# Kernel tuning notes

Measured on AMD Instinct MI355X. Metric: run time of the kernel, lower is better.

## Reference

```python
import jax, jax.numpy as jnp
import numpy as np

NUM_NODES = 4096
IN_DIM = 16
HIDDEN = 64
OUT_DIM = 32
HEADS = 4
NEG_SLOPE = 0.2
NEG_INF = -1e9


def _glorot(key, shape):
    fan_in, fan_out = shape[0], shape[-1]
    lim = jnp.sqrt(6.0 / (fan_in + fan_out))
    return jax.random.uniform(key, shape, jnp.float32, -lim, lim)


def setup_inputs() -> dict:
    key = jax.random.key(0)
    ks = jax.random.split(key, 8)
    B = 2
    return {
        "x": jax.random.normal(ks[0], (B, NUM_NODES, IN_DIM), jnp.float32),
        "embedding": _glorot(ks[1], (NUM_NODES, HIDDEN)),
        "W_proj": _glorot(ks[2], (IN_DIM, HIDDEN)),
        "b_proj": jnp.zeros((HIDDEN,), jnp.float32),
        "W1": _glorot(ks[3], (HIDDEN, HIDDEN)),  # heads=4, 16 per head, concat -> 64
        "att1_src": _glorot(ks[4], (HEADS, HIDDEN // HEADS)),
        "att1_dst": _glorot(ks[5], (HEADS, HIDDEN // HEADS)),
        "b1": jnp.zeros((HIDDEN,), jnp.float32),
        "W2": _glorot(ks[6], (HIDDEN, OUT_DIM)),  # heads=4, 8 per head, concat -> 32
        "att2_src": _glorot(ks[7], (HEADS, OUT_DIM // HEADS)),
        "att2_dst": _glorot(jax.random.fold_in(key, 99), (HEADS, OUT_DIM // HEADS)),
        "b2": jnp.zeros((OUT_DIM,), jnp.float32),
    }


def _gat(x, mask, W, a_src, a_dst, b):
    """Dense masked GAT layer. x: [B,N,Fin], mask: [N,N] bool (shared over batch).

    Equivalent to GATConv over edge list tf.where(adj > 0.5): for each target i,
    softmax over neighbors j of LeakyReLU(a_dst.Wh_i + a_src.Wh_j), aggregate Wh_j.
    """
    B, N, _ = x.shape
    H, F = a_src.shape
    h = (x @ W).reshape(B, N, H, F)                       # [B,N,H,F]
    s_src = jnp.einsum('bnhf,hf->bnh', h, a_src)          # per-source score
    s_dst = jnp.einsum('bnhf,hf->bnh', h, a_dst)          # per-target score
    e = s_dst[:, :, None, :] + s_src[:, None, :, :]       # [B,i,j,H]
    e = jnp.where(e > 0, e, NEG_SLOPE * e)                # LeakyReLU(0.2)
    e = jnp.where(mask[None, :, :, None], e, NEG_INF)
    alpha = jax.nn.softmax(e, axis=2)                     # softmax over neighbors j
    out = jnp.einsum('bijh,bjhf->bihf', alpha, h).reshape(B, N, H * F)
    return out + b


def reference(x, embedding, W_proj, b_proj, W1, att1_src, att1_dst, b1,
              W2, att2_src, att2_dst, b2):
    # AdaptiveAdjacency: cosine similarity of l2-normalized node embeddings
    ne = embedding / jnp.linalg.norm(embedding, axis=-1, keepdims=True)
    adj = ne @ ne.T                                       # [N,N], same for all batch
    mask = adj > 0.5                                      # edge set (incl. self-loops)

    h = x @ W_proj + b_proj                               # Dense proj -> hidden
    h = jax.nn.relu(_gat(h, mask, W1, att1_src, att1_dst, b1))
    return _gat(h, mask, W2, att2_src, att2_dst, b2)
```

## Files before the change

### kernel.cpp

```cpp
#include <hip/hip_runtime.h>
#include <hip/hip_bf16.h>
#include <stdint.h>

#define N_NODES 4096
#define BATCH 2

typedef __attribute__((ext_vector_type(8))) short short8v;
typedef __attribute__((ext_vector_type(4))) unsigned short ushort4v;
typedef __attribute__((ext_vector_type(4))) float f32x4;

#define GLL16(gsrc, ldst) \
    __builtin_amdgcn_global_load_lds((const __attribute__((address_space(1))) void*)(gsrc), \
                                     (__attribute__((address_space(3))) void*)(ldst), 16, 0, 0)

static __device__ inline unsigned short f2bf_rn(float x) {
    unsigned u = __float_as_uint(x);
    unsigned r = (u + 0x7FFFu + ((u >> 16) & 1u)) >> 16;
    return (unsigned short)r;
}
static __device__ inline float bf2f(unsigned short b) {
    return __uint_as_float(((unsigned)b) << 16);
}
static __device__ inline float rl(float v, int k) {
    return __uint_as_float(__builtin_amdgcn_readlane(__float_as_uint(v), k));
}

__global__ __launch_bounds__(256) void k1_kernel(
        const float* __restrict__ emb,
        unsigned short* __restrict__ ne_hi, unsigned short* __restrict__ ne_lo,
        const float* __restrict__ x, const float* __restrict__ Wp,
        const float* __restrict__ bp, const float* __restrict__ W1,
        const float* __restrict__ a1s, const float* __restrict__ a1d,
        float* __restrict__ h1out, float* __restrict__ ssrc, float* __restrict__ sdst) {
    int t = threadIdx.x;
    if (blockIdx.x < 256) {
        int row = blockIdx.x * 16 + (t >> 4);
        int l16 = t & 15;
        float4 v = *(const float4*)&emb[(size_t)row * 64 + l16 * 4];
        float s = v.x * v.x + v.y * v.y + v.z * v.z + v.w * v.w;
#pragma unroll
        for (int m = 8; m >= 1; m >>= 1) s += __shfl_xor(s, m);
        float inv = 1.f / sqrtf(s);
        float n0 = v.x * inv, n1 = v.y * inv, n2 = v.z * inv, n3 = v.w * inv;
        ushort4v h = {f2bf_rn(n0), f2bf_rn(n1), f2bf_rn(n2), f2bf_rn(n3)};
        ushort4v lo = {f2bf_rn(n0 - bf2f(h.x)), f2bf_rn(n1 - bf2f(h.y)),
                       f2bf_rn(n2 - bf2f(h.z)), f2bf_rn(n3 - bf2f(h.w))};
        *(ushort4v*)&ne_hi[(size_t)row * 64 + l16 * 4] = h;
        *(ushort4v*)&ne_lo[(size_t)row * 64 + l16 * 4] = lo;
    } else {
        int b = blockIdx.x - 256;
        int w = t >> 6, l = t & 63;
        int row0 = b * 32 + w * 8;

        float xv[8];
#pragma unroll
        for (int r = 0; r < 8; ++r) xv[r] = x[(size_t)(row0 + r) * 16 + (l & 15)];

        float h0[8];
        float bpv = bp[l];
#pragma unroll
        for (int r = 0; r < 8; ++r) h0[r] = bpv;
#pragma unroll
        for (int k = 0; k < 16; ++k) {
            float wk = Wp[k * 64 + l];
#pragma unroll
            for (int r = 0; r < 8; ++r) h0[r] += rl(xv[r], k) * wk;
        }

        float h1[8] = {0.f, 0.f, 0.f, 0.f, 0.f, 0.f, 0.f, 0.f};
#pragma unroll
        for (int k = 0; k < 64; ++k) {
            float wk = W1[k * 64 + l];
#pragma unroll
            for (int r = 0; r < 8; ++r) h1[r] += rl(h0[r], k) * wk;
        }

        float as_ = a1s[l], ad_ = a1d[l];
#pragma unroll
        for (int r = 0; r < 8; ++r) {
            h1out[(size_t)(row0 + r) * 64 + l] = h1[r];
            float ps = h1[r] * as_, pd = h1[r] * ad_;
#pragma unroll
            for (int m = 8; m >= 1; m >>= 1) {
                ps += __shfl_xor(ps, m);
                pd += __shfl_xor(pd, m);
            }
            if ((l & 15) == 0) {
                ssrc[(size_t)(row0 + r) * 4 + (l >> 4)] = ps;
                sdst[(size_t)(row0 + r) * 4 + (l >> 4)] = pd;
            }
        }
    }
}

__global__ __launch_bounds__(256) void adj_mfma_kernel(
        const unsigned short* __restrict__ hi, const unsigned short* __restrict__ lo,
        unsigned long long* __restrict__ mask) {
    __shared__ unsigned short Ah[128 * 64];
    __shared__ unsigned short Al[128 * 64];
    __shared__ unsigned short Bh[128 * 64];
    __shared__ unsigned short Bl[128 * 64];
    int t = threadIdx.x;
    int w = t >> 6, l = t & 63;
    int i0 = blockIdx.y * 128, j0 = blockIdx.x * 128;

    int cr = l >> 3;
    int slot = (l & 7) ^ cr;
#pragma unroll
    for (int q = 0; q < 4; ++q) {
        int lr = w * 32 + q * 8;
        size_t ga = (size_t)(i0 + lr + cr) * 64 + slot * 8;
        size_t gb = (size_t)(j0 + lr + cr) * 64 + slot * 8;
        GLL16(hi + ga, &Ah[lr * 64]);
        GLL16(lo + ga, &Al[lr * 64]);
        GLL16(hi + gb, &Bh[lr * 64]);
        GLL16(lo + gb, &Bl[lr * 64]);
    }
    __syncthreads();

    int fr = l & 15;
    int s0 = l >> 4;
    int r7 = l & 7;
    short8v aH[2][2], aL[2][2];
#pragma unroll
    for (int rt = 0; rt < 2; ++rt) {
        int base = (w * 32 + rt * 16 + fr) * 64;
        aH[rt][0] = *(const short8v*)&Ah[base + ((s0 ^ r7) << 3)];
        aH[rt][1] = *(const short8v*)&Ah[base + (((s0 + 4) ^ r7) << 3)];
        aL[rt][0] = *(const short8v*)&Al[base + ((s0 ^ r7) << 3)];
        aL[rt][1] = *(const short8v*)&Al[base + (((s0 + 4) ^ r7) << 3)];
    }

    f32x4 acc[2][8];
#pragma unroll
    for (int rt = 0; rt < 2; ++rt)
#pragma unroll
        for (int js = 0; js < 8; ++js) acc[rt][js] = (f32x4){0.f, 0.f, 0.f, 0.f};

#pragma unroll
    for (int js = 0; js < 8; ++js) {
        int bbase = (js * 16 + fr) * 64;
        short8v bH0 = *(const short8v*)&Bh[bbase + ((s0 ^ r7) << 3)];
        short8v bH1 = *(const short8v*)&Bh[bbase + (((s0 + 4) ^ r7) << 3)];
        short8v bL0 = *(const short8v*)&Bl[bbase + ((s0 ^ r7) << 3)];
        short8v bL1 = *(const short8v*)&Bl[bbase + (((s0 + 4) ^ r7) << 3)];
#pragma unroll
        for (int rt = 0; rt < 2; ++rt) {
            f32x4 a = acc[rt][js];
            a = __builtin_amdgcn_mfma_f32_16x16x32_bf16(aH[rt][0], bH0, a, 0, 0, 0);
            a = __builtin_amdgcn_mfma_f32_16x16x32_bf16(aH[rt][1], bH1, a, 0, 0, 0);
            a = __builtin_amdgcn_mfma_f32_16x16x32_bf16(aH[rt][0], bL0, a, 0, 0, 0);
            a = __builtin_amdgcn_mfma_f32_16x16x32_bf16(aH[rt][1], bL1, a, 0, 0, 0);
            a = __builtin_amdgcn_mfma_f32_16x16x32_bf16(aL[rt][0], bH0, a, 0, 0, 0);
            a = __builtin_amdgcn_mfma_f32_16x16x32_bf16(aL[rt][1], bH1, a, 0, 0, 0);
            acc[rt][js] = a;
        }
    }

    int shift = ((l & 15) >> 2) * 16;
    int r = l & 3;
#pragma unroll
    for (int rt = 0; rt < 2; ++rt) {
#pragma unroll
        for (int ws_ = 0; ws_ < 2; ++ws_) {
            unsigned long long w64 = 0;
#pragma unroll
            for (int js2 = 0; js2 < 4; ++js2) {
                f32x4 a = acc[rt][ws_ * 4 + js2];
                unsigned long long c0 = __ballot(a[0] > 0.5f);
                unsigned long long c1 = __ballot(a[1] > 0.5f);
                unsigned long long c2 = __ballot(a[2] > 0.5f);
                unsigned long long c3 = __ballot(a[3] > 0.5f);
                unsigned long long sel = r == 0 ? c0 : r == 1 ? c1 : r == 2 ? c2 : c3;
                w64 |= ((sel >> shift) & 0xFFFFULL) << (js2 * 16);
            }
            if (l < 16)
                mask[(size_t)(i0 + w * 32 + rt * 16 + l) * 64 + blockIdx.x * 2 + ws_] = w64;
        }
    }
}

__global__ __launch_bounds__(256) void agg1_fused_kernel(
        const float* __restrict__ h1, const float* __restrict__ ssrc,
        const float* __restrict__ sdst, const unsigned long long* __restrict__ mask,
        const float* __restrict__ b1, const float* __restrict__ W2,
        const float* __restrict__ a2s, const float* __restrict__ a2d,
        float* __restrict__ h2out, float* __restrict__ s2s, float* __restrict__ s2d) {
    int i = blockIdx.x * 4 + (threadIdx.x >> 6);
    int t = threadIdx.x & 63;
    int hh = t >> 4;

    float sdA = sdst[(size_t)i * 4 + hh];
    float sdB = sdst[(size_t)(i + N_NODES) * 4 + hh];
    unsigned long long myword = mask[(size_t)i * 64 + t];

    float mA = -1e30f, dA = 0.f, aA = 0.f;
    float mB = -1e30f, dB = 0.f, aB = 0.f;
    unsigned long long nz = __ballot(myword != 0ULL);
    while (nz) {
        int lw = __ffsll(nz) - 1;
        nz &= nz - 1;
        unsigned long long wbits = __shfl(myword, lw);
        while (wbits) {
            int bpos = __ffsll(wbits) - 1;
            wbits &= wbits - 1;
            int j = (lw << 6) + bpos;
            float ssA = ssrc[(size_t)j * 4 + hh];
            float ssB = ssrc[(size_t)(j + N_NODES) * 4 + hh];
            float hvA = h1[(size_t)j * 64 + t];
            float hvB = h1[(size_t)(j + N_NODES) * 64 + t];
            float e = sdA + ssA;
            e = e > 0.f ? e : 0.2f * e;
            float mn = fmaxf(mA, e);
            float cf = __expf(mA - mn);
            float wg = __expf(e - mn);
            dA = dA * cf + wg;
            aA = aA * cf + wg * hvA;
            mA = mn;
            e = sdB + ssB;
            e = e > 0.f ? e : 0.2f * e;
            mn = fmaxf(mB, e);
            cf = __expf(mB - mn);
            wg = __expf(e - mn);
            dB = dB * cf + wg;
            aB = aB * cf + wg * hvB;
            mB = mn;
        }
    }
    float b1v = b1[t];
    float oA = fmaxf(aA / dA + b1v, 0.f);
    float oB = fmaxf(aB / dB + b1v, 0.f);

    int l2 = t & 31;
    float acc2A = 0.f, acc2B = 0.f;
#pragma unroll
    for (int k = 0; k < 64; ++k) {
        float wk = W2[k * 32 + l2];
        acc2A += rl(oA, k) * wk;
        acc2B += rl(oB, k) * wk;
    }

    float a2sv = a2s[l2], a2dv = a2d[l2];
    float psA = acc2A * a2sv, pdA = acc2A * a2dv;
    float psB = acc2B * a2sv, pdB = acc2B * a2dv;
#pragma unroll
    for (int mm = 4; mm >= 1; mm >>= 1) {
        psA += __shfl_xor(psA, mm);
        pdA += __shfl_xor(pdA, mm);
        psB += __shfl_xor(psB, mm);
        pdB += __shfl_xor(pdB, mm);
    }
    if (t < 32) {
        h2out[(size_t)i * 32 + t] = acc2A;
        h2out[(size_t)(i + N_NODES) * 32 + t] = acc2B;
        if ((t & 7) == 0) {
            s2s[(size_t)i * 4 + (t >> 3)] = psA;
            s2d[(size_t)i * 4 + (t >> 3)] = pdA;
            s2s[(size_t)(i + N_NODES) * 4 + (t >> 3)] = psB;
            s2d[(size_t)(i + N_NODES) * 4 + (t >> 3)] = pdB;
        }
    }
}

__global__ __launch_bounds__(256) void agg2_kernel(
        const float* __restrict__ hfeat, const float* __restrict__ ssrc,
        const float* __restrict__ sdst, const unsigned long long* __restrict__ mask,
        const float* __restrict__ bias, float* __restrict__ out) {
    int i = blockIdx.x * 4 + (threadIdx.x >> 6);
    int t = threadIdx.x & 63;
    int tt = t & 31;
    int hh = tt >> 3;

    float sdA = sdst[(size_t)i * 4 + hh];
    float sdB = sdst[(size_t)(i + N_NODES) * 4 + hh];
    unsigned long long myword = mask[(size_t)i * 64 + t];

    float mA = -1e30f, dA = 0.f, aA = 0.f;
    float mB = -1e30f, dB = 0.f, aB = 0.f;
    unsigned long long nz = __ballot(myword != 0ULL);
    while (nz) {
        int lw = __ffsll(nz) - 1;
        nz &= nz - 1;
        unsigned long long wbits = __shfl(myword, lw);
        while (wbits) {
            int bpos = __ffsll(wbits) - 1;
            wbits &= wbits - 1;
            int j = (lw << 6) + bpos;
            float ssA = ssrc[(size_t)j * 4 + hh];
            float ssB = ssrc[(size_t)(j + N_NODES) * 4 + hh];
            float hvA = hfeat[(size_t)j * 32 + tt];
            float hvB = hfeat[(size_t)(j + N_NODES) * 32 + tt];
            float e = sdA + ssA;
            e = e > 0.f ? e : 0.2f * e;
            float mn = fmaxf(mA, e);
            float cf = __expf(mA - mn);
            float wg = __expf(e - mn);
            dA = dA * cf + wg;
            aA = aA * cf + wg * hvA;
            mA = mn;
            e = sdB + ssB;
            e = e > 0.f ? e : 0.2f * e;
            mn = fmaxf(mB, e);
            cf = __expf(mB - mn);
            wg = __expf(e - mn);
            dB = dB * cf + wg;
            aB = aB * cf + wg * hvB;
            mB = mn;
        }
    }
    float bv = bias[tt];
    if (t < 32) {
        out[(size_t)i * 32 + tt] = aA / dA + bv;
        out[(size_t)(i + N_NODES) * 32 + tt] = aB / dB + bv;
    }
}

extern "C" void kernel_launch(void* const* d_in, const int* in_sizes, int n_in,
                              void* d_out, int out_size, void* d_ws, size_t ws_size,
                              hipStream_t stream) {
    const float* x   = (const float*)d_in[0];
    const float* emb = (const float*)d_in[1];
    const float* Wp  = (const float*)d_in[2];
    const float* bp  = (const float*)d_in[3];
    const float* W1  = (const float*)d_in[4];
    const float* a1s = (const float*)d_in[5];
    const float* a1d = (const float*)d_in[6];
    const float* b1  = (const float*)d_in[7];
    const float* W2  = (const float*)d_in[8];
    const float* a2s = (const float*)d_in[9];
    const float* a2d = (const float*)d_in[10];
    const float* b2  = (const float*)d_in[11];

    const int ROWS = BATCH * N_NODES;

    char* w = (char*)d_ws;
    unsigned short* ne_hi = (unsigned short*)w;  w += (size_t)N_NODES * 64 * 2;
    unsigned short* ne_lo = (unsigned short*)w;  w += (size_t)N_NODES * 64 * 2;
    unsigned long long* mask = (unsigned long long*)w; w += (size_t)N_NODES * 64 * 8;
    float* h1  = (float*)w;                      w += (size_t)ROWS * 64 * 4;
    float* s1s = (float*)w;                      w += (size_t)ROWS * 4 * 4;
    float* s1d = (float*)w;                      w += (size_t)ROWS * 4 * 4;
    float* h2  = (float*)w;                      w += (size_t)ROWS * 32 * 4;
    float* s2s = (float*)w;                      w += (size_t)ROWS * 4 * 4;
    float* s2d = (float*)w;                      w += (size_t)ROWS * 4 * 4;

    k1_kernel<<<dim3(512), dim3(256), 0, stream>>>(
        emb, ne_hi, ne_lo, x, Wp, bp, W1, a1s, a1d, h1, s1s, s1d);
    adj_mfma_kernel<<<dim3(32, 32), dim3(256), 0, stream>>>(ne_hi, ne_lo, mask);
    agg1_fused_kernel<<<dim3(N_NODES / 4), dim3(256), 0, stream>>>(
        h1, s1s, s1d, mask, b1, W2, a2s, a2d, h2, s2s, s2d);
    agg2_kernel<<<dim3(N_NODES / 4), dim3(256), 0, stream>>>(
        h2, s2s, s2d, mask, b2, (float*)d_out);
}
```

Baseline: 35.47 us.

## Split normalization kernel and fuse projection/GAT1 with K-split adjacency MFMA

Moves the embedding normalization into its own small kernel and merges the dense projection + W1 blocks with the adjacency MFMA tiles into one launch, so the projection work runs alongside the adjacency tiles. The adjacency tile now loads K in two 32-wide halves, which halves shared memory per block and is meant to allow higher occupancy. The cost is an extra barrier per K-step and a serialized loop. The launch count stays the same.

```diff
diff --git a/kernel.cpp b/kernel.cpp
--- a/kernel.cpp
+++ b/kernel.cpp
@@ -25,31 +25,41 @@
     return __uint_as_float(__builtin_amdgcn_readlane(__float_as_uint(v), k));
 }
 
-__global__ __launch_bounds__(256) void k1_kernel(
+__global__ __launch_bounds__(256) void norm_kernel(
         const float* __restrict__ emb,
-        unsigned short* __restrict__ ne_hi, unsigned short* __restrict__ ne_lo,
+        unsigned short* __restrict__ ne_hi, unsigned short* __restrict__ ne_lo) {
+    int t = threadIdx.x;
+    int row = blockIdx.x * 16 + (t >> 4);
+    int l16 = t & 15;
+    float4 v = *(const float4*)&emb[(size_t)row * 64 + l16 * 4];
+    float s = v.x * v.x + v.y * v.y + v.z * v.z + v.w * v.w;
+#pragma unroll
+    for (int m = 8; m >= 1; m >>= 1) s += __shfl_xor(s, m);
+    float inv = 1.f / sqrtf(s);
+    float n0 = v.x * inv, n1 = v.y * inv, n2 = v.z * inv, n3 = v.w * inv;
+    ushort4v h = {f2bf_rn(n0), f2bf_rn(n1), f2bf_rn(n2), f2bf_rn(n3)};
+    ushort4v lo = {f2bf_rn(n0 - bf2f(h.x)), f2bf_rn(n1 - bf2f(h.y)),
+                   f2bf_rn(n2 - bf2f(h.z)), f2bf_rn(n3 - bf2f(h.w))};
+    *(ushort4v*)&ne_hi[(size_t)row * 64 + l16 * 4] = h;
+    *(ushort4v*)&ne_lo[(size_t)row * 64 + l16 * 4] = lo;
+}
+
+__global__ __launch_bounds__(256) void k2_kernel(
+        const unsigned short* __restrict__ hi, const unsigned short* __restrict__ lo,
+        unsigned long long* __restrict__ mask,
         const float* __restrict__ x, const float* __restrict__ Wp,
         const float* __restrict__ bp, const float* __restrict__ W1,
         const float* __restrict__ a1s, const float* __restrict__ a1d,
         float* __restrict__ h1out, float* __restrict__ ssrc, float* __restrict__ sdst) {
+    __shared__ unsigned short Ah[128 * 32];
+    __shared__ unsigned short Al[128 * 32];
+    __shared__ unsigned short Bh[128 * 32];
+    __shared__ unsigned short Bl[128 * 32];
     int t = threadIdx.x;
+    int w = t >> 6, l = t & 63;
+
     if (blockIdx.x < 256) {
-        int row = blockIdx.x * 16 + (t >> 4);
-        int l16 = t & 15;
-        float4 v = *(const float4*)&emb[(size_t)row * 64 + l16 * 4];
-        float s = v.x * v.x + v.y * v.y + v.z * v.z + v.w * v.w;
-#pragma unroll
-        for (int m = 8; m >= 1; m >>= 1) s += __shfl_xor(s, m);
-        float inv = 1.f / sqrtf(s);
-        float n0 = v.x * inv, n1 = v.y * inv, n2 = v.z * inv, n3 = v.w * inv;
-        ushort4v h = {f2bf_rn(n0), f2bf_rn(n1), f2bf_rn(n2), f2bf_rn(n3)};
-        ushort4v lo = {f2bf_rn(n0 - bf2f(h.x)), f2bf_rn(n1 - bf2f(h.y)),
-                       f2bf_rn(n2 - bf2f(h.z)), f2bf_rn(n3 - bf2f(h.w))};
-        *(ushort4v*)&ne_hi[(size_t)row * 64 + l16 * 4] = h;
-        *(ushort4v*)&ne_lo[(size_t)row * 64 + l16 * 4] = lo;
-    } else {
-        int b = blockIdx.x - 256;
-        int w = t >> 6, l = t & 63;
+        int b = blockIdx.x;
         int row0 = b * 32 + w * 8;
 
         float xv[8];
@@ -90,46 +100,16 @@
                 sdst[(size_t)(row0 + r) * 4 + (l >> 4)] = pd;
             }
         }
-    }
-}
-
-__global__ __launch_bounds__(256) void adj_mfma_kernel(
-        const unsigned short* __restrict__ hi, const unsigned short* __restrict__ lo,
-        unsigned long long* __restrict__ mask) {
-    __shared__ unsigned short Ah[128 * 64];
-    __shared__ unsigned short Al[128 * 64];
-    __shared__ unsigned short Bh[128 * 64];
-    __shared__ unsigned short Bl[128 * 64];
-    int t = threadIdx.x;
-    int w = t >> 6, l = t & 63;
-    int i0 = blockIdx.y * 128, j0 = blockIdx.x * 128;
-
-    int cr = l >> 3;
-    int slot = (l & 7) ^ cr;
-#pragma unroll
-    for (int q = 0; q < 4; ++q) {
-        int lr = w * 32 + q * 8;
-        size_t ga = (size_t)(i0 + lr + cr) * 64 + slot * 8;
-        size_t gb = (size_t)(j0 + lr + cr) * 64 + slot * 8;
-        GLL16(hi + ga, &Ah[lr * 64]);
-        GLL16(lo + ga, &Al[lr * 64]);
-        GLL16(hi + gb, &Bh[lr * 64]);
-        GLL16(lo + gb, &Bl[lr * 64]);
-    }
-    __syncthreads();
+        return;
+    }
+
+    int tile = blockIdx.x - 256;
+    int bi = tile >> 5, bj = tile & 31;
+    int i0 = bi * 128, j0 = bj * 128;
 
     int fr = l & 15;
     int s0 = l >> 4;
-    int r7 = l & 7;
-    short8v aH[2][2], aL[2][2];
-#pragma unroll
-    for (int rt = 0; rt < 2; ++rt) {
-        int base = (w * 32 + rt * 16 + fr) * 64;
-        aH[rt][0] = *(const short8v*)&Ah[base + ((s0 ^ r7) << 3)];
-        aH[rt][1] = *(const short8v*)&Ah[base + (((s0 + 4) ^ r7) << 3)];
-        aL[rt][0] = *(const short8v*)&Al[base + ((s0 ^ r7) << 3)];
-        aL[rt][1] = *(const short8v*)&Al[base + (((s0 + 4) ^ r7) << 3)];
-    }
+    int sw = (s0 ^ (fr & 3)) << 3;
 
     f32x4 acc[2][8];
 #pragma unroll
@@ -137,24 +117,46 @@
 #pragma unroll
         for (int js = 0; js < 8; ++js) acc[rt][js] = (f32x4){0.f, 0.f, 0.f, 0.f};
 
-#pragma unroll
-    for (int js = 0; js < 8; ++js) {
-        int bbase = (js * 16 + fr) * 64;
-        short8v bH0 = *(const short8v*)&Bh[bbase + ((s0 ^ r7) << 3)];
-        short8v bH1 = *(const short8v*)&Bh[bbase + (((s0 + 4) ^ r7) << 3)];
-        short8v bL0 = *(const short8v*)&Bl[bbase + ((s0 ^ r7) << 3)];
-        short8v bL1 = *(const short8v*)&Bl[bbase + (((s0 + 4) ^ r7) << 3)];
+    int cr = l >> 2;
+    int sl = (l & 3) ^ (cr & 3);
+
+#pragma unroll 1
+    for (int ks = 0; ks < 2; ++ks) {
+#pragma unroll
+        for (int q = 0; q < 2; ++q) {
+            int lr = w * 32 + q * 16;
+            size_t ga = (size_t)(i0 + lr + cr) * 64 + ks * 32 + sl * 8;
+            size_t gb = (size_t)(j0 + lr + cr) * 64 + ks * 32 + sl * 8;
+            GLL16(hi + ga, &Ah[lr * 32]);
+            GLL16(lo + ga, &Al[lr * 32]);
+            GLL16(hi + gb, &Bh[lr * 32]);
+            GLL16(lo + gb, &Bl[lr * 32]);
+        }
+        __syncthreads();
+
+        short8v aH[2], aL[2];
 #pragma unroll
         for (int rt = 0; rt < 2; ++rt) {
-            f32x4 a = acc[rt][js];
-            a = __builtin_amdgcn_mfma_f32_16x16x32_bf16(aH[rt][0], bH0, a, 0, 0, 0);
-            a = __builtin_amdgcn_mfma_f32_16x16x32_bf16(aH[rt][1], bH1, a, 0, 0, 0);
-            a = __builtin_amdgcn_mfma_f32_16x16x32_bf16(aH[rt][0], bL0, a, 0, 0, 0);
-            a = __builtin_amdgcn_mfma_f32_16x16x32_bf16(aH[rt][1], bL1, a, 0, 0, 0);
-            a = __builtin_amdgcn_mfma_f32_16x16x32_bf16(aL[rt][0], bH0, a, 0, 0, 0);
-            a = __builtin_amdgcn_mfma_f32_16x16x32_bf16(aL[rt][1], bH1, a, 0, 0, 0);
-            acc[rt][js] = a;
-        }
+            int base = (w * 32 + rt * 16 + fr) * 32 + sw;
+            aH[rt] = *(const short8v*)&Ah[base];
+            aL[rt] = *(const short8v*)&Al[base];
+        }
+
+#pragma unroll
+        for (int js = 0; js < 8; ++js) {
+            int bbase = (js * 16 + fr) * 32 + sw;
+            short8v bH = *(const short8v*)&Bh[bbase];
+            short8v bL = *(const short8v*)&Bl[bbase];
+#pragma unroll
+            for (int rt = 0; rt < 2; ++rt) {
+                f32x4 a = acc[rt][js];
+                a = __builtin_amdgcn_mfma_f32_16x16x32_bf16(aH[rt], bH, a, 0, 0, 0);
+                a = __builtin_amdgcn_mfma_f32_16x16x32_bf16(aH[rt], bL, a, 0, 0, 0);
+                a = __builtin_amdgcn_mfma_f32_16x16x32_bf16(aL[rt], bH, a, 0, 0, 0);
+                acc[rt][js] = a;
+            }
+        }
+        if (ks == 0) __syncthreads();
     }
 
     int shift = ((l & 15) >> 2) * 16;
@@ -175,7 +177,7 @@
                 w64 |= ((sel >> shift) & 0xFFFFULL) << (js2 * 16);
             }
             if (l < 16)
-                mask[(size_t)(i0 + w * 32 + rt * 16 + l) * 64 + blockIdx.x * 2 + ws_] = w64;
+                mask[(size_t)(i0 + w * 32 + rt * 16 + l) * 64 + bj * 2 + ws_] = w64;
         }
     }
 }
@@ -344,9 +346,9 @@
     float* s2s = (float*)w;                      w += (size_t)ROWS * 4 * 4;
     float* s2d = (float*)w;                      w += (size_t)ROWS * 4 * 4;
 
-    k1_kernel<<<dim3(512), dim3(256), 0, stream>>>(
-        emb, ne_hi, ne_lo, x, Wp, bp, W1, a1s, a1d, h1, s1s, s1d);
-    adj_mfma_kernel<<<dim3(32, 32), dim3(256), 0, stream>>>(ne_hi, ne_lo, mask);
+    norm_kernel<<<dim3(256), dim3(256), 0, stream>>>(emb, ne_hi, ne_lo);
+    k2_kernel<<<dim3(1280), dim3(256), 0, stream>>>(
+        ne_hi, ne_lo, mask, x, Wp, bp, W1, a1s, a1d, h1, s1s, s1d);
     agg1_fused_kernel<<<dim3(N_NODES / 4), dim3(256), 0, stream>>>(
         h1, s1s, s1d, mask, b1, W2, a2s, a2d, h2, s2s, s2d);
     agg2_kernel<<<dim3(N_NODES / 4), dim3(256), 0, stream>>>(
```

After: 33.66 us. -5.1%, faster.
